# Kernel tuning notes

Measured on AMD Instinct MI355X. Metric: run time of the kernel, lower is better.

## Reference

```python
import jax, jax.numpy as jnp
import numpy as np

B, T, D, H, L = 256, 512, 200, 320, 3

def setup_inputs() -> dict:
    key = jax.random.key(0)
    ks = jax.random.split(key, 5)
    # small scale on weights for numerical stability (orthogonal-init-like magnitude)
    return {
        "x": jax.random.normal(ks[0], (B, T, D), jnp.float32),
        "hidden0": jnp.zeros((L, B, H), jnp.float32),
        "running_mean": jnp.zeros((D,), jnp.float32),
        "running_var": jnp.ones((D,), jnp.float32),
        "w_ih0": jax.random.normal(ks[1], (3 * H, D), jnp.float32) * 0.05,
        "w_ih_rest": jax.random.normal(ks[2], (L - 1, 3 * H, H), jnp.float32) * 0.05,
        "w_hh": jax.random.normal(ks[3], (L, 3 * H, H), jnp.float32) * 0.05,
        "b_ih": jnp.zeros((L, 3 * H), jnp.float32),
        "b_hh": jnp.zeros((L, 3 * H), jnp.float32),
        "ln_gamma": jnp.ones((L, 3, H), jnp.float32),
        "ln_beta": jnp.zeros((L, 3, H), jnp.float32),
    }

def _layernorm(z, g, b, eps=1e-5):
    mu = z.mean(-1, keepdims=True)
    var = ((z - mu) ** 2).mean(-1, keepdims=True)
    return (z - mu) / jnp.sqrt(var + eps) * g + b

def _cell(inp, h, W_ih, B_ih, W_hh, B_hh, G, Bt):
    gi = inp @ W_ih.T + B_ih          # [B, 3H]
    gh = h @ W_hh.T + B_hh            # [B, 3H]
    ir, iu, inw = jnp.split(gi, 3, axis=-1)
    hr, hu, hn = jnp.split(gh, 3, axis=-1)
    r = jax.nn.sigmoid(_layernorm(ir + hr, G[0], Bt[0]))
    u = jax.nn.sigmoid(_layernorm(iu + hu, G[1], Bt[1]))
    n = jnp.tanh(_layernorm(inw + r * hn, G[2], Bt[2]))
    return (1.0 - u) * n + u * h

def reference(x, hidden0, running_mean, running_var, w_ih0, w_ih_rest, w_hh,
              b_ih, b_hh, ln_gamma, ln_beta):
    # eval-mode RunningStatsNorm + clamp
    x_norm = jnp.clip((x - running_mean) / jnp.sqrt(running_var + 1e-8), -10.0, 10.0)
    w_ih_list = [w_ih0] + [w_ih_rest[i] for i in range(w_ih_rest.shape[0])]
    n_layers = len(w_ih_list)

    def step(h, xt):  # h: [L,B,H], xt: [B,D]
        inp = xt
        new_h = []
        for i in range(n_layers):
            inp = _cell(inp, h[i], w_ih_list[i], b_ih[i], w_hh[i], b_hh[i],
                        ln_gamma[i], ln_beta[i])
            new_h.append(inp)
        return jnp.stack(new_h), inp

    final_h, outs = jax.lax.scan(step, hidden0, jnp.swapaxes(x_norm, 0, 1))
    output = jnp.swapaxes(outs, 0, 1)  # [B, T, H]
    return output, final_h
```

## Files before the change

### kernel.cpp

```cpp
#include <hip/hip_runtime.h>
#include <hip/hip_fp16.h>

#define B_   256
#define T_   512
#define D_   200
#define H_   320
#define L_   3
#define G3_  960
#define BH_  (B_*H_)
#define BTH_ (B_*T_*H_)

#define GR_   8
#define RPG_  32
#define CPB_  48
#define NCG_  20
#define SPG_  60
#define NP2_  24
#define NBLK  512
#define NTHR  256
#define KIP0  224
#define WSTR  648

typedef _Float16 half8 __attribute__((ext_vector_type(8)));
typedef float    f32x4 __attribute__((ext_vector_type(4)));

#define OFF_Z     0
#define SZ_Z      (L_*B_*G3_)
#define OFF_HN    (OFF_Z + SZ_Z)
#define SZ_HN     (L_*B_*H_)
#define OFF_STF   (OFF_HN + SZ_HN)
#define SZ_STF_F  ((L_*BH_)/2)
#define OFF_BAR   (OFF_STF + SZ_STF_F)
#define FLAG_STR  32
#define FB_OFF    2048
#define GRP_STR   4096
#define TCK_OFF   (GR_*GRP_STR)
#define BAR_WORDS (GR_*GRP_STR + 256)

__device__ __forceinline__ float sigmoidf_(float v) {
    return 1.0f / (1.0f + __expf(-v));
}

__device__ __forceinline__ float wredsum(float v) {
#pragma unroll
    for (int m = 32; m > 0; m >>= 1) v += __shfl_xor(v, m, 64);
    return v;
}

__device__ __forceinline__ half8 h8zero() {
    half8 a;
#pragma unroll
    for (int j = 0; j < 8; ++j) a[j] = (_Float16)0.f;
    return a;
}

__device__ __forceinline__ void l2st(unsigned* p, unsigned v) {
    __hip_atomic_store(p, v, __ATOMIC_RELAXED, __HIP_MEMORY_SCOPE_WORKGROUP);
}
__device__ __forceinline__ unsigned l2ticket(unsigned* p) {
    return __hip_atomic_fetch_add(p, 1u, __ATOMIC_RELAXED, __HIP_MEMORY_SCOPE_WORKGROUP);
}

__device__ __forceinline__ void bar_signal(unsigned* flags, int idx, int tid,
                                           unsigned token) {
    __syncthreads();
    if (tid == 0) l2st(&flags[idx*FLAG_STR], token);
}
__device__ __forceinline__ void bar_wait(unsigned* flags, int nflags, int tid,
                                         unsigned token) {
    if (tid < 64) {
        for (;;) {
            asm volatile("buffer_inv" ::: "memory");
            unsigned v = token;
            if (tid < nflags) v = ((volatile unsigned*)flags)[tid*FLAG_STR];
            if (__all((int)(v - token) >= 0)) break;
            __builtin_amdgcn_s_sleep(1);
        }
    }
    __syncthreads();
    asm volatile("buffer_inv" ::: "memory");
}

__device__ __forceinline__ void load_weights(int l, int colbase, int tid,
        const float* __restrict__ wih0, const float* __restrict__ wihr,
        const float* __restrict__ whh,  const float* __restrict__ rmean,
        const float* __restrict__ rvar,
        _Float16 (*w)[WSTR], float (*nrm)[KIP0])
{
    for (int e = tid; e < CPB_*WSTR; e += NTHR) ((_Float16*)w)[e] = (_Float16)0.f;
    if (l == 0) for (int e = tid; e < 2*KIP0; e += NTHR) ((float*)nrm)[e] = 0.f;
    __syncthreads();
    const int KI  = (l == 0) ? D_ : H_;
    const int KIP = (l == 0) ? KIP0 : H_;
    for (int e = tid; e < CPB_*KI; e += NTHR) {
        int c = e / KI, k = e - c*KI;
        float v = (l == 0) ? wih0[(size_t)(colbase + c)*D_ + k]
                           : wihr[((size_t)(l-1)*G3_ + colbase + c)*H_ + k];
        w[c][k] = (_Float16)v;
    }
    for (int e = tid; e < CPB_*H_; e += NTHR) {
        int c = e / H_, k = e - c*H_;
        w[c][KIP + k] = (_Float16)whh[((size_t)l*G3_ + colbase + c)*H_ + k];
    }
    if (l == 0) {
        for (int k = tid; k < D_; k += NTHR) {
            nrm[0][k] = rmean[k];
            nrm[1][k] = rsqrtf(rvar[k] + 1e-8f);
        }
    }
    __syncthreads();
}

template<int KTI, bool L0>
__device__ __forceinline__ void phase1_work(int g, int l, int t, int colbase, int tid,
        const float* __restrict__ x, const _Float16* __restrict__ stf,
        const float* __restrict__ bih, const float* __restrict__ bhh,
        float* __restrict__ zbuf, float* __restrict__ hnbuf,
        const _Float16 (*w)[WSTR], const float (*nrm)[KIP0])
{
    const int wid  = tid >> 6;
    const int lane = tid & 63;
    const int nr   = lane & 15;
    const int grp  = lane >> 4;
    const int mb   = g*RPG_ + wid*16;
    constexpr int KIP = KTI * 32;

    half8 aI[KTI];
    if (L0) {
#pragma unroll
        for (int kt = 0; kt < KTI; ++kt) {
            if (kt == KTI-1 && grp > 0) { aI[kt] = h8zero(); continue; }
            const int k0 = kt*32 + grp*8;
            const float* xr = &x[((size_t)(mb + nr)*T_ + t)*D_ + k0];
            float xv[8];
            *(float4*)&xv[0] = *(const float4*)xr;
            *(float4*)&xv[4] = *(const float4*)(xr + 4);
#pragma unroll
            for (int j = 0; j < 8; ++j) {
                float nv = (xv[j] - nrm[0][k0+j]) * nrm[1][k0+j];
                aI[kt][j] = (_Float16)fminf(fmaxf(nv, -10.f), 10.f);
            }
        }
    } else {
        const _Float16* srcI = &stf[(size_t)(l-1)*BH_ + (size_t)(mb + nr)*H_ + grp*8];
#pragma unroll
        for (int kt = 0; kt < KTI; ++kt) aI[kt] = *(const half8*)(srcI + kt*32);
    }
    half8 aH[10];
    {
        const _Float16* srcH = &stf[(size_t)l*BH_ + (size_t)(mb + nr)*H_ + grp*8];
#pragma unroll
        for (int kt = 0; kt < 10; ++kt) aH[kt] = *(const half8*)(srcH + kt*32);
    }

    f32x4 accI[3], accH[3];
#pragma unroll
    for (int nt = 0; nt < 3; ++nt) {
#pragma unroll
        for (int r = 0; r < 4; ++r) { accI[nt][r] = 0.f; accH[nt][r] = 0.f; }
    }

#pragma unroll
    for (int kt = 0; kt < KTI; ++kt) {
        const int k0 = kt*32 + grp*8;
#pragma unroll
        for (int nt = 0; nt < 3; ++nt) {
            half8 bf = *(const half8*)&w[nt*16 + nr][k0];
            accI[nt] = __builtin_amdgcn_mfma_f32_16x16x32_f16(aI[kt], bf, accI[nt], 0, 0, 0);
        }
    }
#pragma unroll
    for (int kt = 0; kt < 10; ++kt) {
        const int k0 = kt*32 + grp*8;
#pragma unroll
        for (int nt = 0; nt < 3; ++nt) {
            half8 bf = *(const half8*)&w[nt*16 + nr][KIP + k0];
            accH[nt] = __builtin_amdgcn_mfma_f32_16x16x32_f16(aH[kt], bf, accH[nt], 0, 0, 0);
        }
    }

#pragma unroll
    for (int nt = 0; nt < 3; ++nt) {
        const int col = colbase + nt*16 + nr;
        const float bi = bih[l*G3_ + col];
        const float bh = bhh[l*G3_ + col];
        const bool ru = (colbase + nt*16) < 2*H_;
#pragma unroll
        for (int r = 0; r < 4; ++r) {
            const int m = mb + grp*4 + r;
            const size_t zi = ((size_t)l*B_ + m)*G3_ + col;
            if (ru) {
                zbuf[zi] = accI[nt][r] + accH[nt][r] + bi + bh;
            } else {
                zbuf[zi] = accI[nt][r] + bi;
                hnbuf[((size_t)l*B_ + m)*H_ + (col - 2*H_)] = accH[nt][r] + bh;
            }
        }
    }
}

__device__ __forceinline__ void phase1_dispatch(int g, int l, int t, int colbase, int tid,
        const float* x, const _Float16* stf, const float* bih, const float* bhh,
        float* zbuf, float* hnbuf, const _Float16 (*w)[WSTR], const float (*nrm)[KIP0])
{
    if ((tid >> 6) >= 2) return;
    if (l == 0) phase1_work<7,  true >(g, l, t, colbase, tid, x, stf, bih, bhh, zbuf, hnbuf, w, nrm);
    else        phase1_work<10, false>(g, l, t, colbase, tid, x, stf, bih, bhh, zbuf, hnbuf, w, nrm);
}

__device__ __forceinline__ void phase2_work(int g, int tau, int wv, int lane,
        const float* __restrict__ lng, const float* __restrict__ lnb,
        float* hreg, _Float16* __restrict__ stf,
        const float* __restrict__ zbuf, const float* __restrict__ hnbuf,
        float* __restrict__ out)
{
    if (wv >= L_*RPG_) return;
    const int l2  = wv >> 5;
    const int row = wv & 31;
    const int b2  = g*RPG_ + row;
    const int t2  = tau - l2;
    if (t2 < 0 || t2 >= T_) return;

    const float* zrow  = &zbuf[((size_t)l2*B_ + b2)*G3_];
    const float* hnrow = &hnbuf[((size_t)l2*B_ + b2)*H_];
    _Float16*    frow  = &stf[(size_t)l2*BH_ + (size_t)b2*H_];

    float zr[5], zu[5], zn[5], hn[5];
#pragma unroll
    for (int i = 0; i < 5; ++i) {
        const int j = lane + i*64;
        zr[i] = zrow[j];
        zu[i] = zrow[320 + j];
        zn[i] = zrow[640 + j];
        hn[i] = hnrow[j];
    }
    const float inv320 = 1.0f/320.0f;
    float s  = zr[0]+zr[1]+zr[2]+zr[3]+zr[4];
    float mu = wredsum(s) * inv320;
    float vs = 0.f;
#pragma unroll
    for (int i = 0; i < 5; ++i) { float d = zr[i]-mu; vs += d*d; }
    float inv = rsqrtf(wredsum(vs)*inv320 + 1e-5f);
    float r[5];
#pragma unroll
    for (int i = 0; i < 5; ++i) {
        const int j = lane + i*64;
        r[i] = sigmoidf_((zr[i]-mu)*inv * lng[(l2*3+0)*H_ + j] + lnb[(l2*3+0)*H_ + j]);
    }
    s  = zu[0]+zu[1]+zu[2]+zu[3]+zu[4];
    mu = wredsum(s) * inv320;
    vs = 0.f;
#pragma unroll
    for (int i = 0; i < 5; ++i) { float d = zu[i]-mu; vs += d*d; }
    inv = rsqrtf(wredsum(vs)*inv320 + 1e-5f);
    float u[5];
#pragma unroll
    for (int i = 0; i < 5; ++i) {
        const int j = lane + i*64;
        u[i] = sigmoidf_((zu[i]-mu)*inv * lng[(l2*3+1)*H_ + j] + lnb[(l2*3+1)*H_ + j]);
    }
    float z2[5];
#pragma unroll
    for (int i = 0; i < 5; ++i) z2[i] = zn[i] + r[i]*hn[i];
    s  = z2[0]+z2[1]+z2[2]+z2[3]+z2[4];
    mu = wredsum(s) * inv320;
    vs = 0.f;
#pragma unroll
    for (int i = 0; i < 5; ++i) { float d = z2[i]-mu; vs += d*d; }
    inv = rsqrtf(wredsum(vs)*inv320 + 1e-5f);
#pragma unroll
    for (int i = 0; i < 5; ++i) {
        const int j = lane + i*64;
        float nv = tanhf((z2[i]-mu)*inv * lng[(l2*3+2)*H_ + j] + lnb[(l2*3+2)*H_ + j]);
        float hv = (1.0f - u[i])*nv + u[i]*hreg[i];
        hreg[i] = hv;
        unsigned hb = (unsigned)__builtin_bit_cast(unsigned short, (_Float16)hv);
        unsigned ob = (unsigned)__shfl_xor((int)hb, 1, 64);
        if ((lane & 1) == 0)
            ((unsigned*)frow)[j >> 1] = (hb & 0xffffu) | (ob << 16);
        if (l2 == 2)    out[((size_t)b2*T_ + t2)*H_ + j] = hv;
        if (t2 == T_-1) out[(size_t)BTH_ + ((size_t)l2*B_ + b2)*H_ + j] = hv;
    }
}

__global__ void k_init(const float* __restrict__ h0, float* __restrict__ ws) {
    _Float16*  stf = (_Float16*)(ws + OFF_STF);
    unsigned*  bar = (unsigned*)(ws + OFF_BAR);
    int gt = blockIdx.x*blockDim.x + threadIdx.x;
    for (int i = gt; i < BAR_WORDS; i += gridDim.x*blockDim.x) bar[i] = 0u;
    for (int i = gt; i < L_*BH_; i += gridDim.x*blockDim.x)
        stf[i] = (_Float16)h0[i];
}

__launch_bounds__(NTHR, 2)
__global__ void gru_pers_kernel(const float* __restrict__ x,
                                const float* __restrict__ h0,
                                const float* __restrict__ rmean,
                                const float* __restrict__ rvar,
                                const float* __restrict__ wih0,
                                const float* __restrict__ wihr,
                                const float* __restrict__ whh,
                                const float* __restrict__ bih,
                                const float* __restrict__ bhh,
                                const float* __restrict__ lng,
                                const float* __restrict__ lnb,
                                float* __restrict__ out,
                                float* __restrict__ ws)
{
    float*     zbuf  = ws + OFF_Z;
    float*     hnbuf = ws + OFF_HN;
    _Float16*  stf   = (_Float16*)(ws + OFF_STF);
    unsigned*  bar   = (unsigned*)(ws + OFF_BAR);

    const int tid = threadIdx.x;

    unsigned myxcd;
    asm volatile("s_getreg_b32 %0, hwreg(HW_REG_XCC_ID)" : "=s"(myxcd));
    myxcd &= 7u;
    __shared__ unsigned sh_slot;
    if (tid == 0) sh_slot = l2ticket(&bar[TCK_OFF + myxcd*32]);
    __syncthreads();
    const unsigned slot = sh_slot;
    if (slot >= (unsigned)SPG_) return;

    const int g   = (int)myxcd;
    const int idx = (int)slot;
    const int l   = idx / NCG_;
    const int cgp = idx - l*NCG_;
    const int colbase = cgp * CPB_;
    const bool p2blk = (idx < NP2_);

    unsigned* flagsA = bar + g*GRP_STR;
    unsigned* flagsB = bar + g*GRP_STR + FB_OFF;

    __shared__ _Float16 w_lds[CPB_][WSTR];
    __shared__ float    nrm_lds[2][KIP0];

    load_weights(l, colbase, tid, wih0, wihr, whh, rmean, rvar, w_lds, nrm_lds);

    const int wid  = tid >> 6;
    const int lane = tid & 63;
    const int wv   = idx*4 + wid;

    float hreg[5] = {0.f, 0.f, 0.f, 0.f, 0.f};
    if (wv < L_*RPG_) {
        const int l2 = wv >> 5, row = wv & 31, b2 = g*RPG_ + row;
#pragma unroll
        for (int i = 0; i < 5; ++i)
            hreg[i] = h0[(size_t)l2*BH_ + (size_t)b2*H_ + lane + i*64];
    }

    for (int tau = 0; tau < T_ + L_ - 1; ++tau) {
        const unsigned tok = (unsigned)(tau + 1);
        const int t = tau - l;
        if (t >= 0 && t < T_)
            phase1_dispatch(g, l, t, colbase, tid, x, stf, bih, bhh,
                            zbuf, hnbuf, w_lds, nrm_lds);
        bar_signal(flagsA, idx, tid, tok);
        if (p2blk) {
            bar_wait(flagsA, SPG_, tid, tok);
            phase2_work(g, tau, wv, lane, lng, lnb, hreg, stf, zbuf, hnbuf, out);
            bar_signal(flagsB, idx, tid, tok);
        }
        bar_wait(flagsB, NP2_, tid, tok);
    }
}

extern "C" void kernel_launch(void* const* d_in, const int* in_sizes, int n_in,
                              void* d_out, int out_size, void* d_ws, size_t ws_size,
                              hipStream_t stream) {
    (void)in_sizes; (void)n_in; (void)out_size; (void)ws_size;
    const float* x     = (const float*)d_in[0];
    const float* h0    = (const float*)d_in[1];
    const float* rmean = (const float*)d_in[2];
    const float* rvar  = (const float*)d_in[3];
    const float* wih0  = (const float*)d_in[4];
    const float* wihr  = (const float*)d_in[5];
    const float* whh   = (const float*)d_in[6];
    const float* bih   = (const float*)d_in[7];
    const float* bhh   = (const float*)d_in[8];
    const float* lng   = (const float*)d_in[9];
    const float* lnb   = (const float*)d_in[10];
    float* out = (float*)d_out;
    float* ws  = (float*)d_ws;

    k_init<<<dim3(240), dim3(NTHR), 0, stream>>>(h0, ws);
    gru_pers_kernel<<<dim3(NBLK), dim3(NTHR), 0, stream>>>(
        x, h0, rmean, rvar, wih0, wihr, whh, bih, bhh, lng, lnb, out, ws);
}
```

Before: 5.163 ms.

## Prefetch next-step x inputs and defer output stores past barrier signal

Layer-0 blocks now load and normalize the next timestep's x slice right after signaling the phase-1 barrier, so that global load latency overlaps with barrier waiting instead of sitting on the critical path. Phase-2 waves keep their layernorm gamma/beta values in registers for the whole loop instead of reloading them every step. The global output stores are moved after the phase-2 barrier signal so other blocks can proceed sooner. The cost is higher register pressure from the prefetched half8 array and the gamma/beta registers, which could reduce occupancy under launch_bounds(256,2).

```diff
diff --git a/kernel.cpp b/kernel.cpp
--- a/kernel.cpp
+++ b/kernel.cpp
@@ -113,10 +113,10 @@
 
 template<int KTI, bool L0>
 __device__ __forceinline__ void phase1_work(int g, int l, int t, int colbase, int tid,
-        const float* __restrict__ x, const _Float16* __restrict__ stf,
+        const _Float16* __restrict__ stf,
         const float* __restrict__ bih, const float* __restrict__ bhh,
         float* __restrict__ zbuf, float* __restrict__ hnbuf,
-        const _Float16 (*w)[WSTR], const float (*nrm)[KIP0])
+        const _Float16 (*w)[WSTR], const half8* aIpre)
 {
     const int wid  = tid >> 6;
     const int lane = tid & 63;
@@ -128,19 +128,7 @@
     half8 aI[KTI];
     if (L0) {
 #pragma unroll
-        for (int kt = 0; kt < KTI; ++kt) {
-            if (kt == KTI-1 && grp > 0) { aI[kt] = h8zero(); continue; }
-            const int k0 = kt*32 + grp*8;
-            const float* xr = &x[((size_t)(mb + nr)*T_ + t)*D_ + k0];
-            float xv[8];
-            *(float4*)&xv[0] = *(const float4*)xr;
-            *(float4*)&xv[4] = *(const float4*)(xr + 4);
-#pragma unroll
-            for (int j = 0; j < 8; ++j) {
-                float nv = (xv[j] - nrm[0][k0+j]) * nrm[1][k0+j];
-                aI[kt][j] = (_Float16)fminf(fmaxf(nv, -10.f), 10.f);
-            }
-        }
+        for (int kt = 0; kt < KTI; ++kt) aI[kt] = aIpre[kt];
     } else {
         const _Float16* srcI = &stf[(size_t)(l-1)*BH_ + (size_t)(mb + nr)*H_ + grp*8];
 #pragma unroll
@@ -199,28 +187,12 @@
     }
 }
 
-__device__ __forceinline__ void phase1_dispatch(int g, int l, int t, int colbase, int tid,
-        const float* x, const _Float16* stf, const float* bih, const float* bhh,
-        float* zbuf, float* hnbuf, const _Float16 (*w)[WSTR], const float (*nrm)[KIP0])
+__device__ __forceinline__ void phase2_core(int l2, int b2, int lane,
+        const float* g0r, const float* c0r, const float* g1r, const float* c1r,
+        const float* g2r, const float* c2r,
+        float* hreg, float* hv5, _Float16* __restrict__ stf,
+        const float* __restrict__ zbuf, const float* __restrict__ hnbuf)
 {
-    if ((tid >> 6) >= 2) return;
-    if (l == 0) phase1_work<7,  true >(g, l, t, colbase, tid, x, stf, bih, bhh, zbuf, hnbuf, w, nrm);
-    else        phase1_work<10, false>(g, l, t, colbase, tid, x, stf, bih, bhh, zbuf, hnbuf, w, nrm);
-}
-
-__device__ __forceinline__ void phase2_work(int g, int tau, int wv, int lane,
-        const float* __restrict__ lng, const float* __restrict__ lnb,
-        float* hreg, _Float16* __restrict__ stf,
-        const float* __restrict__ zbuf, const float* __restrict__ hnbuf,
-        float* __restrict__ out)
-{
-    if (wv >= L_*RPG_) return;
-    const int l2  = wv >> 5;
-    const int row = wv & 31;
-    const int b2  = g*RPG_ + row;
-    const int t2  = tau - l2;
-    if (t2 < 0 || t2 >= T_) return;
-
     const float* zrow  = &zbuf[((size_t)l2*B_ + b2)*G3_];
     const float* hnrow = &hnbuf[((size_t)l2*B_ + b2)*H_];
     _Float16*    frow  = &stf[(size_t)l2*BH_ + (size_t)b2*H_];
@@ -243,10 +215,8 @@
     float inv = rsqrtf(wredsum(vs)*inv320 + 1e-5f);
     float r[5];
 #pragma unroll
-    for (int i = 0; i < 5; ++i) {
-        const int j = lane + i*64;
-        r[i] = sigmoidf_((zr[i]-mu)*inv * lng[(l2*3+0)*H_ + j] + lnb[(l2*3+0)*H_ + j]);
-    }
+    for (int i = 0; i < 5; ++i)
+        r[i] = sigmoidf_((zr[i]-mu)*inv * g0r[i] + c0r[i]);
     s  = zu[0]+zu[1]+zu[2]+zu[3]+zu[4];
     mu = wredsum(s) * inv320;
     vs = 0.f;
@@ -255,10 +225,8 @@
     inv = rsqrtf(wredsum(vs)*inv320 + 1e-5f);
     float u[5];
 #pragma unroll
-    for (int i = 0; i < 5; ++i) {
-        const int j = lane + i*64;
-        u[i] = sigmoidf_((zu[i]-mu)*inv * lng[(l2*3+1)*H_ + j] + lnb[(l2*3+1)*H_ + j]);
-    }
+    for (int i = 0; i < 5; ++i)
+        u[i] = sigmoidf_((zu[i]-mu)*inv * g1r[i] + c1r[i]);
     float z2[5];
 #pragma unroll
     for (int i = 0; i < 5; ++i) z2[i] = zn[i] + r[i]*hn[i];
@@ -271,15 +239,14 @@
 #pragma unroll
     for (int i = 0; i < 5; ++i) {
         const int j = lane + i*64;
-        float nv = tanhf((z2[i]-mu)*inv * lng[(l2*3+2)*H_ + j] + lnb[(l2*3+2)*H_ + j]);
+        float nv = tanhf((z2[i]-mu)*inv * g2r[i] + c2r[i]);
         float hv = (1.0f - u[i])*nv + u[i]*hreg[i];
         hreg[i] = hv;
+        hv5[i]  = hv;
         unsigned hb = (unsigned)__builtin_bit_cast(unsigned short, (_Float16)hv);
         unsigned ob = (unsigned)__shfl_xor((int)hb, 1, 64);
         if ((lane & 1) == 0)
             ((unsigned*)frow)[j >> 1] = (hb & 0xffffu) | (ob << 16);
-        if (l2 == 2)    out[((size_t)b2*T_ + t2)*H_ + j] = hv;
-        if (t2 == T_-1) out[(size_t)BTH_ + ((size_t)l2*B_ + b2)*H_ + j] = hv;
     }
 }
 
@@ -341,26 +308,74 @@
     const int wid  = tid >> 6;
     const int lane = tid & 63;
     const int wv   = idx*4 + wid;
-
+    const int nr   = lane & 15;
+    const int grp  = lane >> 4;
+
+    const bool p2act = p2blk && (wv < L_*RPG_);
+    const int  l2 = wv >> 5, row = wv & 31, b2 = g*RPG_ + row;
     float hreg[5] = {0.f, 0.f, 0.f, 0.f, 0.f};
-    if (wv < L_*RPG_) {
-        const int l2 = wv >> 5, row = wv & 31, b2 = g*RPG_ + row;
-#pragma unroll
-        for (int i = 0; i < 5; ++i)
-            hreg[i] = h0[(size_t)l2*BH_ + (size_t)b2*H_ + lane + i*64];
-    }
+    float g0r[5], c0r[5], g1r[5], c1r[5], g2r[5], c2r[5];
+    if (p2act) {
+#pragma unroll
+        for (int i = 0; i < 5; ++i) {
+            const int j = lane + i*64;
+            hreg[i] = h0[(size_t)l2*BH_ + (size_t)b2*H_ + j];
+            g0r[i] = lng[(l2*3+0)*H_ + j];  c0r[i] = lnb[(l2*3+0)*H_ + j];
+            g1r[i] = lng[(l2*3+1)*H_ + j];  c1r[i] = lnb[(l2*3+1)*H_ + j];
+            g2r[i] = lng[(l2*3+2)*H_ + j];  c2r[i] = lnb[(l2*3+2)*H_ + j];
+        }
+    }
+
+    half8 aIx[7];
+    const bool xload = (l == 0) && (wid < 2);
+    const int  mbx   = g*RPG_ + wid*16;
+    auto prefetch_x = [&](int t) {
+        if (!xload || t >= T_) return;
+#pragma unroll
+        for (int kt = 0; kt < 7; ++kt) {
+            if (kt == 6 && grp > 0) { aIx[kt] = h8zero(); continue; }
+            const int k0 = kt*32 + grp*8;
+            const float* xr = &x[((size_t)(mbx + nr)*T_ + t)*D_ + k0];
+            float xv[8];
+            *(float4*)&xv[0] = *(const float4*)xr;
+            *(float4*)&xv[4] = *(const float4*)(xr + 4);
+#pragma unroll
+            for (int j = 0; j < 8; ++j) {
+                float nv = (xv[j] - nrm_lds[0][k0+j]) * nrm_lds[1][k0+j];
+                aIx[kt][j] = (_Float16)fminf(fmaxf(nv, -10.f), 10.f);
+            }
+        }
+    };
+    prefetch_x(0);
 
     for (int tau = 0; tau < T_ + L_ - 1; ++tau) {
         const unsigned tok = (unsigned)(tau + 1);
         const int t = tau - l;
-        if (t >= 0 && t < T_)
-            phase1_dispatch(g, l, t, colbase, tid, x, stf, bih, bhh,
-                            zbuf, hnbuf, w_lds, nrm_lds);
+        if (t >= 0 && t < T_ && wid < 2) {
+            if (l == 0) phase1_work<7,  true >(g, l, t, colbase, tid, stf, bih, bhh,
+                                               zbuf, hnbuf, w_lds, aIx);
+            else        phase1_work<10, false>(g, l, t, colbase, tid, stf, bih, bhh,
+                                               zbuf, hnbuf, w_lds, nullptr);
+        }
         bar_signal(flagsA, idx, tid, tok);
+        prefetch_x(t + 1);
+        const int t2 = tau - l2;
+        const bool act = p2act && t2 >= 0 && t2 < T_;
+        float hv5[5];
         if (p2blk) {
             bar_wait(flagsA, SPG_, tid, tok);
-            phase2_work(g, tau, wv, lane, lng, lnb, hreg, stf, zbuf, hnbuf, out);
+            if (act)
+                phase2_core(l2, b2, lane, g0r, c0r, g1r, c1r, g2r, c2r,
+                            hreg, hv5, stf, zbuf, hnbuf);
             bar_signal(flagsB, idx, tid, tok);
+            if (act) {
+#pragma unroll
+                for (int i = 0; i < 5; ++i) {
+                    const int j = lane + i*64;
+                    if (l2 == 2)    out[((size_t)b2*T_ + t2)*H_ + j] = hv5[i];
+                    if (t2 == T_-1) out[(size_t)BTH_ + ((size_t)l2*B_ + b2)*H_ + j] = hv5[i];
+                }
+            }
         }
         bar_wait(flagsB, NP2_, tid, tok);
     }
```

New measurement: 7.265 ms. 1.41x slower.
